# Kernel optimization log

Hardware: AMD Instinct MI355X
Metric: run time of the kernel (lower is better)

Reference implementation:

```python
import math
import jax, jax.numpy as jnp
import numpy as np

BS, N, D, H = 4, 512, 1024, 16
HD = D // H


def setup_inputs() -> dict:
    key = jax.random.key(0)
    ks = jax.random.split(key, 12)
    s = 1.0 / math.sqrt(D)
    return {
        "x": jax.random.normal(ks[0], (BS, N, D), jnp.float32),
        "r": jax.random.normal(ks[1], (BS, 3, N, N), jnp.float32),
        "bias": jax.random.normal(ks[2], (BS, H, N, N), jnp.float32),
        "mask": jax.random.randint(ks[3], (BS, 1, N, N), 0, 2, jnp.int32),
        "wq": jax.random.normal(ks[4], (D, D), jnp.float32) * s,
        "bq": jnp.zeros((D,), jnp.float32),
        "wk": jax.random.normal(ks[5], (D, D), jnp.float32) * s,
        "bk": jnp.zeros((D,), jnp.float32),
        "wv": jax.random.normal(ks[6], (D, D), jnp.float32) * s,
        "bv": jnp.zeros((D,), jnp.float32),
        "wo": jax.random.normal(ks[7], (D, 1), jnp.float32) * s,
        "bo": jnp.zeros((1,), jnp.float32),
    }


def reference(x, r, bias, mask, wq, bq, wk, bk, wv, bv, wo, bo):
    bs, n, d = x.shape
    # projections -> (bs, h, n, hd)
    q = (x @ wq + bq).reshape(bs, n, H, HD).transpose(0, 2, 1, 3)
    k = (x @ wk + bk).reshape(bs, n, H, HD).transpose(0, 2, 1, 3)
    v = (x @ wv + bv).reshape(bs, n, H, HD).transpose(0, 2, 1, 3)
    logits = jnp.einsum("bhid,bhjd->bhij", q, k) / math.sqrt(HD) + bias
    logits = jnp.where(mask == 0, jnp.float32(-1e9), logits)
    w = jax.nn.softmax(logits, axis=-1)  # (bs,h,n,n)
    # o[b,i,c,h,d] = sum_j r[b,c,i,j] * w[b,h,i,j] * v[b,h,j,d]
    o = jnp.einsum("bcij,bhij,bhjd->bichd", r, w, v)
    o = o.reshape(bs, n, 3, d)
    force = o @ wo + bo  # (bs, n, 3, 1)
    return force
```

## Files before the change

kernel.cpp:

```cpp
#include <hip/hip_runtime.h>
#include <stdint.h>

#define BSZ 4
#define NSEQ 512
#define DMOD 1024
#define NH 16
#define HD 64

typedef __attribute__((ext_vector_type(8))) short bf16x8;
typedef __attribute__((ext_vector_type(4))) float f32x4;

__device__ __forceinline__ unsigned short f2bf(float f) {
    union { float f; uint32_t u; } v; v.f = f;
    uint32_t u = v.u;
    u += 0x7FFFu + ((u >> 16) & 1u);
    return (unsigned short)(u >> 16);
}

__device__ __forceinline__ void gload_lds16(const unsigned short* g, unsigned short* l) {
    __builtin_amdgcn_global_load_lds(
        (const __attribute__((address_space(1))) void*)g,
        (__attribute__((address_space(3))) void*)l, 16, 0, 0);
}

#define LGKM_BAR() do { \
    asm volatile("s_waitcnt lgkmcnt(0)" ::: "memory"); \
    __builtin_amdgcn_sched_barrier(0); \
    __builtin_amdgcn_s_barrier(); \
    __builtin_amdgcn_sched_barrier(0); } while (0)

__global__ __launch_bounds__(256) void k_prep(
        const float* __restrict__ x, const float* __restrict__ wq, const float* __restrict__ wk,
        const float* __restrict__ wv, const float* __restrict__ bv, const float* __restrict__ wo,
        unsigned short* __restrict__ xb, unsigned short* __restrict__ wqt,
        unsigned short* __restrict__ wkt, float* __restrict__ wv2t, float* __restrict__ bv2) {
    __shared__ float t[32][33];
    int bx = blockIdx.x, tid = threadIdx.x;
    if (bx < 2048) {
        int i = bx * 256 + tid;
        float4 v = ((const float4*)x)[i];
        ushort4 o; o.x = f2bf(v.x); o.y = f2bf(v.y); o.z = f2bf(v.z); o.w = f2bf(v.w);
        ((ushort4*)xb)[i] = o;
    } else if (bx < 4096) {
        int g = bx - 2048; int z = g >> 10; g &= 1023;
        const float* src = z ? wk : wq;
        unsigned short* dst = z ? wkt : wqt;
        int be = (g & 31) * 32, bc = (g >> 5) * 32;
        int tx = tid & 31, ty = tid >> 5;
        #pragma unroll
        for (int yy = 0; yy < 32; yy += 8)
            t[ty + yy][tx] = src[(size_t)(be + ty + yy) * DMOD + bc + tx];
        __syncthreads();
        #pragma unroll
        for (int yy = 0; yy < 32; yy += 8)
            dst[(size_t)(bc + ty + yy) * DMOD + be + tx] = f2bf(t[tx][ty + yy]);
    } else {
        int g = bx - 4096;
        int grp = tid >> 6, l = tid & 63;
        int e = g * 4 + grp;
        float out = 0.f;
        #pragma unroll
        for (int it = 0; it < 16; ++it) {
            float v = wv[(size_t)e * DMOD + it * 64 + l] * wo[it * 64 + l];
            #pragma unroll
            for (int off = 1; off < 64; off <<= 1) v += __shfl_xor(v, off, 64);
            if (l == it) out = v;
        }
        if (l < 16) wv2t[l * DMOD + e] = out;
        if (g == 0 && grp == 0) {
            float ob = 0.f;
            #pragma unroll
            for (int it = 0; it < 16; ++it) {
                float v = bv[it * 64 + l] * wo[it * 64 + l];
                #pragma unroll
                for (int off = 1; off < 64; off <<= 1) v += __shfl_xor(v, off, 64);
                if (l == it) ob = v;
            }
            if (l < 16) bv2[l] = ob;
        }
    }
}

__global__ __launch_bounds__(256, 3) void k_mid(
        const float* __restrict__ x, const float* __restrict__ wv2t, const float* __restrict__ bv2,
        const unsigned short* __restrict__ xb, const unsigned short* __restrict__ wqt,
        const unsigned short* __restrict__ wkt, const float* __restrict__ bq,
        const float* __restrict__ bk, float* __restrict__ u,
        unsigned short* __restrict__ qT, unsigned short* __restrict__ kT) {
    __shared__ unsigned short lA[128 * 64];
    __shared__ unsigned short lB[128 * 64];
    int bx = blockIdx.x, tid = threadIdx.x;
    if (bx >= 256) {
        int wave = (bx - 256) * 4 + (tid >> 6);
        int l = tid & 63;
        int b = wave >> 9, j = wave & 511;
        const float* xr = x + (size_t)(b * NSEQ + j) * DMOD;
        float p[16];
        #pragma unroll
        for (int h = 0; h < 16; ++h) p[h] = 0.f;
        for (int it = 0; it < 16; ++it) {
            int e = l + it * 64;
            float xv = xr[e];
            #pragma unroll
            for (int h = 0; h < 16; ++h) p[h] += xv * wv2t[h * DMOD + e];
        }
        #pragma unroll
        for (int h = 0; h < 16; ++h) {
            #pragma unroll
            for (int off = 1; off < 64; off <<= 1) p[h] += __shfl_xor(p[h], off, 64);
        }
        float out = 0.f;
        #pragma unroll
        for (int h = 0; h < 16; ++h) if (l == h) out = p[h] + bv2[h];
        if (l < 16) u[(b * 16 + l) * NSEQ + j] = out;
        return;
    }
    int g = bx;
    int mt = g & 15, nt8 = (g >> 4) & 7, z = g >> 7;
    const unsigned short* Wt = z ? wkt : wqt;
    const float* bias = z ? bk : bq;
    unsigned short* outT = z ? kT : qT;
    float scale = z ? 1.f : 0.125f;
    int m0 = mt * 128, n0 = nt8 * 128;
    int w = tid >> 6, lane = tid & 63;
    int wr = w >> 1, wc = w & 1;
    int quad = lane >> 4, cs = lane & 15;
    int l8 = lane >> 3, l7 = lane & 7;
    int sg = l7 ^ l8;

    f32x4 acc[4][4];
    #pragma unroll
    for (int mi = 0; mi < 4; ++mi)
        #pragma unroll
        for (int ni = 0; ni < 4; ++ni) acc[mi][ni] = (f32x4){0.f, 0.f, 0.f, 0.f};

    for (int kc = 0; kc < 16; ++kc) {
        int k0 = kc * 64;
        #pragma unroll
        for (int q = 0; q < 4; ++q) {
            int row = w * 32 + q * 8 + l8;
            gload_lds16(xb + (size_t)(m0 + row) * DMOD + k0 + sg * 8,
                        &lA[(w * 32 + q * 8) * 64]);
            gload_lds16(Wt + (size_t)(n0 + row) * DMOD + k0 + sg * 8,
                        &lB[(w * 32 + q * 8) * 64]);
        }
        __syncthreads();
        #pragma unroll
        for (int ks = 0; ks < 2; ++ks) {
            bf16x8 af[4], bfr[4];
            #pragma unroll
            for (int mi = 0; mi < 4; ++mi) {
                int row = wr * 64 + mi * 16 + cs;
                int gq = (ks * 4 + quad) ^ (row & 7);
                af[mi] = *(const bf16x8*)&lA[row * 64 + gq * 8];
            }
            #pragma unroll
            for (int ni = 0; ni < 4; ++ni) {
                int row = wc * 64 + ni * 16 + cs;
                int gq = (ks * 4 + quad) ^ (row & 7);
                bfr[ni] = *(const bf16x8*)&lB[row * 64 + gq * 8];
            }
            #pragma unroll
            for (int mi = 0; mi < 4; ++mi)
                #pragma unroll
                for (int ni = 0; ni < 4; ++ni)
                    acc[mi][ni] = __builtin_amdgcn_mfma_f32_16x16x32_bf16(
                        af[mi], bfr[ni], acc[mi][ni], 0, 0, 0);
        }
        __syncthreads();
    }
    #pragma unroll
    for (int ni = 0; ni < 4; ++ni) {
        int n = n0 + wc * 64 + ni * 16 + cs;
        int h = n >> 6, d = n & 63;
        float bvv = bias[n];
        #pragma unroll
        for (int mi = 0; mi < 4; ++mi) {
            #pragma unroll
            for (int rr = 0; rr < 4; ++rr) {
                int mg = m0 + wr * 64 + mi * 16 + quad * 4 + rr;
                int b = mg >> 9, i = mg & 511;
                outT[(size_t)((b * 16 + h) * NSEQ + i) * HD + d] =
                    f2bf((acc[mi][ni][rr] + bvv) * scale);
            }
        }
    }
}

__global__ __launch_bounds__(512, 2) void k_attn(
        const unsigned short* __restrict__ qT, const unsigned short* __restrict__ kT,
        const float* __restrict__ bias, const int* __restrict__ mask,
        const float* __restrict__ u, const float* __restrict__ r,
        float* __restrict__ spart, float* __restrict__ P) {
    __shared__ float rT4[2][16 * 64 * 4];
    int tid = threadIdx.x;
    int w = tid >> 6, lane = tid & 63;
    int quad = lane >> 4, col = lane & 15;
    int it = blockIdx.x, bz = blockIdx.y;
    int b = bz >> 1, hg = bz & 1;
    int i0 = it * 16;
    int h = hg * 8 + w;
    int bh = b * 16 + h;

    const float* rbase = r + (size_t)b * 3 * NSEQ * NSEQ;
    const int* mrow = mask + (size_t)b * NSEQ * NSEQ;
    const float* brow = bias + (size_t)bh * NSEQ * NSEQ;
    const unsigned short* kbh = kT + (size_t)bh * NSEQ * HD;
    const float* ub = u + (size_t)bh * NSEQ;

    const unsigned short* qbase = qT + ((size_t)(bh * NSEQ + i0 + col)) * HD + quad * 8;
    bf16x8 a0 = *(const bf16x8*)qbase;
    bf16x8 a1 = *(const bf16x8*)(qbase + 32);

    bf16x8 kf0[2][4], kf1[2][4];
    float uvv[2][4], bvv[2][16];
    float s0[2][2], s1[2][2], s2[2][2], smf[2][2];

    auto prefetch = [&](int jc, int pb) {
        int j0 = jc * 64;
        #pragma unroll
        for (int jt = 0; jt < 4; ++jt) {
            const unsigned short* kb = kbh + ((size_t)(j0 + jt * 16 + col)) * HD + quad * 8;
            kf0[pb][jt] = *(const bf16x8*)kb;
            kf1[pb][jt] = *(const bf16x8*)(kb + 32);
            uvv[pb][jt] = ub[j0 + jt * 16 + col];
            int j = j0 + jt * 16 + col;
            #pragma unroll
            for (int rr = 0; rr < 4; ++rr) {
                int i = i0 + quad * 4 + rr;
                bvv[pb][jt * 4 + rr] = __builtin_nontemporal_load(&brow[(size_t)i * NSEQ + j]);
            }
        }
        #pragma unroll
        for (int t = 0; t < 2; ++t) {
            int slot = t * 512 + tid;
            int il = slot >> 6, jl = slot & 63;
            size_t off = (size_t)(i0 + il) * NSEQ + j0 + jl;
            s0[pb][t] = rbase[off];
            s1[pb][t] = rbase[(size_t)NSEQ * NSEQ + off];
            s2[pb][t] = rbase[2 * (size_t)NSEQ * NSEQ + off];
            smf[pb][t] = (float)mrow[off];
        }
    };
    auto pack = [&](int pb) {
        #pragma unroll
        for (int t = 0; t < 2; ++t) {
            int slot = t * 512 + tid;
            float4 pk; pk.x = s0[pb][t]; pk.y = s1[pb][t]; pk.z = s2[pb][t]; pk.w = smf[pb][t];
            *(float4*)&rT4[pb][slot * 4] = pk;
        }
    };

    prefetch(0, 0);
    pack(0);
    LGKM_BAR();

    #pragma unroll 8
    for (int jc = 0; jc < 8; ++jc) {
        int cur = jc & 1, nxt = cur ^ 1;
        if (jc < 7) prefetch(jc + 1, nxt);

        float sp[4]  = {0.f, 0.f, 0.f, 0.f};
        float pc0[4] = {0.f, 0.f, 0.f, 0.f};
        float pc1[4] = {0.f, 0.f, 0.f, 0.f};
        float pc2[4] = {0.f, 0.f, 0.f, 0.f};
        const float* rbuf = rT4[cur];
        #pragma unroll
        for (int jt = 0; jt < 4; ++jt) {
            f32x4 acc = (f32x4){0.f, 0.f, 0.f, 0.f};
            acc = __builtin_amdgcn_mfma_f32_16x16x32_bf16(a0, kf0[cur][jt], acc, 0, 0, 0);
            acc = __builtin_amdgcn_mfma_f32_16x16x32_bf16(a1, kf1[cur][jt], acc, 0, 0, 0);
            float uv = uvv[cur][jt];
            int jl = jt * 16 + col;
            #pragma unroll
            for (int rr = 0; rr < 4; ++rr) {
                int il = quad * 4 + rr;
                float4 v = *(const float4*)&rbuf[(il * 64 + jl) * 4];
                float lg = acc[rr] + bvv[cur][jt * 4 + rr];
                float e = __expf(lg) * v.w;
                sp[rr] += e;
                float eu = e * uv;
                pc0[rr] += eu * v.x;
                pc1[rr] += eu * v.y;
                pc2[rr] += eu * v.z;
            }
        }
        #pragma unroll
        for (int rr = 0; rr < 4; ++rr) {
            #pragma unroll
            for (int off = 1; off < 16; off <<= 1) {
                sp[rr]  += __shfl_xor(sp[rr], off, 64);
                pc0[rr] += __shfl_xor(pc0[rr], off, 64);
                pc1[rr] += __shfl_xor(pc1[rr], off, 64);
                pc2[rr] += __shfl_xor(pc2[rr], off, 64);
            }
        }
        if (col == 0) {
            #pragma unroll
            for (int rr = 0; rr < 4; ++rr) {
                int il = quad * 4 + rr;
                spart[((size_t)bh * NSEQ + i0 + il) * 8 + jc] = sp[rr];
                size_t pb2 = ((((size_t)bh * 32 + it) * 16 + il) * 8 + jc) * 3;
                P[pb2 + 0] = pc0[rr];
                P[pb2 + 1] = pc1[rr];
                P[pb2 + 2] = pc2[rr];
            }
        }
        if (jc < 7) { pack(nxt); LGKM_BAR(); }
    }
}

__global__ __launch_bounds__(256) void k_final(
        const float* __restrict__ spart, const float* __restrict__ P,
        const float* __restrict__ bo, float* __restrict__ out) {
    __shared__ float part[4][16][3];
    int bx = blockIdx.x;
    int b = bx >> 5, it = bx & 31;
    int tid = threadIdx.x;
    int il = tid & 15, h = tid >> 4;
    int w = tid >> 6;
    int bh = b * 16 + h;
    int i = it * 16 + il;
    const float* sprow = spart + ((size_t)bh * NSEQ + i) * 8;
    float4 sa = *(const float4*)sprow;
    float4 sb = *(const float4*)(sprow + 4);
    float s = sa.x + sa.y + sa.z + sa.w + sb.x + sb.y + sb.z + sb.w;
    float sinv = (s > 0.f) ? 1.f / s : 0.f;
    const float* pbase = P + (((size_t)bh * 32 + it) * 16 + il) * 24;
    float f[3] = {0.f, 0.f, 0.f};
    #pragma unroll
    for (int q = 0; q < 6; ++q) {
        float4 v = *(const float4*)(pbase + q * 4);
        f[(q * 4 + 0) % 3] += v.x;
        f[(q * 4 + 1) % 3] += v.y;
        f[(q * 4 + 2) % 3] += v.z;
        f[(q * 4 + 3) % 3] += v.w;
    }
    f[0] *= sinv; f[1] *= sinv; f[2] *= sinv;
    #pragma unroll
    for (int c = 0; c < 3; ++c) {
        f[c] += __shfl_xor(f[c], 16, 64);
        f[c] += __shfl_xor(f[c], 32, 64);
    }
    if ((tid & 48) == 0) {
        part[w][il][0] = f[0]; part[w][il][1] = f[1]; part[w][il][2] = f[2];
    }
    __syncthreads();
    if (tid < 16) {
        float bov = bo[0];
        float o0 = part[0][tid][0] + part[1][tid][0] + part[2][tid][0] + part[3][tid][0];
        float o1 = part[0][tid][1] + part[1][tid][1] + part[2][tid][1] + part[3][tid][1];
        float o2 = part[0][tid][2] + part[1][tid][2] + part[2][tid][2] + part[3][tid][2];
        size_t row = (size_t)b * NSEQ + it * 16 + tid;
        out[row * 3 + 0] = o0 + bov;
        out[row * 3 + 1] = o1 + bov;
        out[row * 3 + 2] = o2 + bov;
    }
}

extern "C" void kernel_launch(void* const* d_in, const int* in_sizes, int n_in,
                              void* d_out, int out_size, void* d_ws, size_t ws_size,
                              hipStream_t stream) {
    const float* x    = (const float*)d_in[0];
    const float* rr   = (const float*)d_in[1];
    const float* bias = (const float*)d_in[2];
    const int*   mask = (const int*)d_in[3];
    const float* wq   = (const float*)d_in[4];
    const float* bq   = (const float*)d_in[5];
    const float* wk   = (const float*)d_in[6];
    const float* bk   = (const float*)d_in[7];
    const float* wv   = (const float*)d_in[8];
    const float* bv   = (const float*)d_in[9];
    const float* wo   = (const float*)d_in[10];
    const float* bo   = (const float*)d_in[11];
    float* out = (float*)d_out;

    char* ws = (char*)d_ws;
    unsigned short* xb    = (unsigned short*)(ws + 0);
    unsigned short* wqt   = (unsigned short*)(ws + 4194304);
    unsigned short* wkt   = (unsigned short*)(ws + 6291456);
    float*          wv2t  = (float*)(ws + 8388608);
    float*          bv2   = (float*)(ws + 8454144);
    float*          u     = (float*)(ws + 8454400);
    unsigned short* qT    = (unsigned short*)(ws + 8585472);
    unsigned short* kT    = (unsigned short*)(ws + 12779776);
    float*          spart = (float*)(ws + 16974080);
    float*          P     = (float*)(ws + 18022656);

    k_prep<<<4352, 256, 0, stream>>>(x, wq, wk, wv, bv, wo, xb, wqt, wkt, wv2t, bv2);
    k_mid<<<768, 256, 0, stream>>>(x, wv2t, bv2, xb, wqt, wkt, bq, bk, u, qT, kT);
    k_attn<<<dim3(32, 8), 512, 0, stream>>>(qT, kT, bias, mask, u, rr, spart, P);
    k_final<<<128, 256, 0, stream>>>(spart, P, bo, out);
}
```

Measured before the change: 196.2 us.

## Load r and mask directly per lane in attention kernel, dropping LDS staging

The attention kernel no longer stages r and mask through a double-buffered LDS tile with barriers. Each lane now loads the r and mask values it needs straight from global memory, in its MFMA output layout, inside the current iteration. This removes the LDS writes, the LDS reads and the block barriers, and the mask becomes a select instead of a multiply. In exchange the loads are strided (16 columns per row, 4 rows per lane) and are not prefetched a chunk ahead, so their latency is exposed. The launch-bounds minimum-blocks hint of 2 is also dropped.

Result: no change. 198.9 us (+1.4%).

```diff
diff --git a/kernel.cpp b/kernel.cpp
--- a/kernel.cpp
+++ b/kernel.cpp
@@ -22,12 +22,6 @@
         (const __attribute__((address_space(1))) void*)g,
         (__attribute__((address_space(3))) void*)l, 16, 0, 0);
 }
-
-#define LGKM_BAR() do { \
-    asm volatile("s_waitcnt lgkmcnt(0)" ::: "memory"); \
-    __builtin_amdgcn_sched_barrier(0); \
-    __builtin_amdgcn_s_barrier(); \
-    __builtin_amdgcn_sched_barrier(0); } while (0)
 
 __global__ __launch_bounds__(256) void k_prep(
         const float* __restrict__ x, const float* __restrict__ wq, const float* __restrict__ wk,
@@ -187,12 +181,11 @@
     }
 }
 
-__global__ __launch_bounds__(512, 2) void k_attn(
+__global__ __launch_bounds__(512) void k_attn(
         const unsigned short* __restrict__ qT, const unsigned short* __restrict__ kT,
         const float* __restrict__ bias, const int* __restrict__ mask,
         const float* __restrict__ u, const float* __restrict__ r,
         float* __restrict__ spart, float* __restrict__ P) {
-    __shared__ float rT4[2][16 * 64 * 4];
     int tid = threadIdx.x;
     int w = tid >> 6, lane = tid & 63;
     int quad = lane >> 4, col = lane & 15;
@@ -214,7 +207,6 @@
 
     bf16x8 kf0[2][4], kf1[2][4];
     float uvv[2][4], bvv[2][16];
-    float s0[2][2], s1[2][2], s2[2][2], smf[2][2];
 
     auto prefetch = [&](int jc, int pb) {
         int j0 = jc * 64;
@@ -231,58 +223,51 @@
                 bvv[pb][jt * 4 + rr] = __builtin_nontemporal_load(&brow[(size_t)i * NSEQ + j]);
             }
         }
-        #pragma unroll
-        for (int t = 0; t < 2; ++t) {
-            int slot = t * 512 + tid;
-            int il = slot >> 6, jl = slot & 63;
-            size_t off = (size_t)(i0 + il) * NSEQ + j0 + jl;
-            s0[pb][t] = rbase[off];
-            s1[pb][t] = rbase[(size_t)NSEQ * NSEQ + off];
-            s2[pb][t] = rbase[2 * (size_t)NSEQ * NSEQ + off];
-            smf[pb][t] = (float)mrow[off];
-        }
     };
-    auto pack = [&](int pb) {
-        #pragma unroll
-        for (int t = 0; t < 2; ++t) {
-            int slot = t * 512 + tid;
-            float4 pk; pk.x = s0[pb][t]; pk.y = s1[pb][t]; pk.z = s2[pb][t]; pk.w = smf[pb][t];
-            *(float4*)&rT4[pb][slot * 4] = pk;
-        }
-    };
 
     prefetch(0, 0);
-    pack(0);
-    LGKM_BAR();
 
     #pragma unroll 8
     for (int jc = 0; jc < 8; ++jc) {
         int cur = jc & 1, nxt = cur ^ 1;
         if (jc < 7) prefetch(jc + 1, nxt);
+        int j0 = jc * 64;
+
+        float rv0[16], rv1[16], rv2[16];
+        int mv[16];
+        #pragma unroll
+        for (int jt = 0; jt < 4; ++jt) {
+            int j = j0 + jt * 16 + col;
+            #pragma unroll
+            for (int rr = 0; rr < 4; ++rr) {
+                int i = i0 + quad * 4 + rr;
+                size_t off = (size_t)i * NSEQ + j;
+                rv0[jt * 4 + rr] = rbase[off];
+                rv1[jt * 4 + rr] = rbase[(size_t)NSEQ * NSEQ + off];
+                rv2[jt * 4 + rr] = rbase[2 * (size_t)NSEQ * NSEQ + off];
+                mv[jt * 4 + rr] = mrow[off];
+            }
+        }
 
         float sp[4]  = {0.f, 0.f, 0.f, 0.f};
         float pc0[4] = {0.f, 0.f, 0.f, 0.f};
         float pc1[4] = {0.f, 0.f, 0.f, 0.f};
         float pc2[4] = {0.f, 0.f, 0.f, 0.f};
-        const float* rbuf = rT4[cur];
         #pragma unroll
         for (int jt = 0; jt < 4; ++jt) {
             f32x4 acc = (f32x4){0.f, 0.f, 0.f, 0.f};
             acc = __builtin_amdgcn_mfma_f32_16x16x32_bf16(a0, kf0[cur][jt], acc, 0, 0, 0);
             acc = __builtin_amdgcn_mfma_f32_16x16x32_bf16(a1, kf1[cur][jt], acc, 0, 0, 0);
             float uv = uvv[cur][jt];
-            int jl = jt * 16 + col;
-            #pragma unroll
-            for (int rr = 0; rr < 4; ++rr) {
-                int il = quad * 4 + rr;
-                float4 v = *(const float4*)&rbuf[(il * 64 + jl) * 4];
+            #pragma unroll
+            for (int rr = 0; rr < 4; ++rr) {
                 float lg = acc[rr] + bvv[cur][jt * 4 + rr];
-                float e = __expf(lg) * v.w;
+                float e = (mv[jt * 4 + rr] == 0) ? 0.f : __expf(lg);
                 sp[rr] += e;
                 float eu = e * uv;
-                pc0[rr] += eu * v.x;
-                pc1[rr] += eu * v.y;
-                pc2[rr] += eu * v.z;
+                pc0[rr] += eu * rv0[jt * 4 + rr];
+                pc1[rr] += eu * rv1[jt * 4 + rr];
+                pc2[rr] += eu * rv2[jt * 4 + rr];
             }
         }
         #pragma unroll
@@ -306,7 +291,6 @@
                 P[pb2 + 2] = pc2[rr];
             }
         }
-        if (jc < 7) { pack(nxt); LGKM_BAR(); }
     }
 }
 
```
